# Performance work log

Hardware: AMD Instinct MI355X
Metric: run time of the kernel (lower is better)

## Reference

```python
import jax, jax.numpy as jnp
import numpy as np

B, T, IN, H = 64, 1024, 512, 512

def setup_inputs() -> dict:
    key = jax.random.key(0)
    k1, k2, k3, k4, k5 = jax.random.split(key, 5)
    s_w = 1.0 / np.sqrt(IN)
    s_u = 1.0 / np.sqrt(H)
    return {
        "X": jax.random.normal(k1, (B, T, IN), dtype=jnp.float32),
        "h_0": jnp.zeros((B, H), dtype=jnp.float32),
        "W_w": jax.random.uniform(k2, (H, IN), jnp.float32, -s_w, s_w),
        "W_b": jax.random.uniform(k3, (H,), jnp.float32, -s_w, s_w),
        "U_w": jax.random.uniform(k4, (H, H), jnp.float32, -s_u, s_u),
        "U_b": jax.random.uniform(k5, (H,), jnp.float32, -s_u, s_u),
    }

def reference(X, h_0, W_w, W_b, U_w, U_b):
    # Precompute input projection for all timesteps: [B,T,H]
    Wx = jnp.einsum('bti,hi->bth', X, W_w) + W_b
    Wx_t = jnp.swapaxes(Wx, 0, 1)  # [T,B,H] for scan

    def step(h_prev, wx_t):
        h_t = jnp.tanh(wx_t + h_prev @ U_w.T + U_b)
        return h_t, h_t

    _, H_seq = jax.lax.scan(step, h_0, Wx_t)  # [T,B,H]
    return jnp.swapaxes(H_seq, 0, 1)  # [B,T,H]
```

## Files before the change

kernel.cpp:

```cpp
#include <hip/hip_runtime.h>
#include <cstdint>
#include <cstddef>


#define T_STEPS 1024

using f16 = _Float16;
typedef f16  f16x2 __attribute__((ext_vector_type(2)));
typedef f16  f16x8 __attribute__((ext_vector_type(8)));
typedef float f32x4 __attribute__((ext_vector_type(4)));

#if __has_builtin(__builtin_amdgcn_fdot2)
#define FDOT2(a, b, c) __builtin_amdgcn_fdot2((a), (b), (c), false)
#else
static __device__ __forceinline__ float FDOT2(f16x2 a, f16x2 b, float c) {
    return c + (float)a[0] * (float)b[0] + (float)a[1] * (float)b[1];
}
#endif

static __device__ __forceinline__ f16x2 bcast_pair(int v) {
    return __builtin_bit_cast(f16x2, v);
}

__global__ __launch_bounds__(256, 2)
void gemm_wx(const float* __restrict__ X, const float* __restrict__ W,
             const float* __restrict__ Wb, float* __restrict__ out) {
    __shared__ __align__(16) char Al[128 * 128];
    __shared__ __align__(16) char Bl[128 * 128];

    const int tid  = threadIdx.x;
    const int lane = tid & 63;
    const int wid  = tid >> 6;
    const int wm   = wid & 1;
    const int wn   = wid >> 1;
    const int m0   = blockIdx.x * 128;
    const int n0   = blockIdx.y * 128;

    f32x4 acc[4][4] = {};

    for (int kt = 0; kt < 512; kt += 64) {
        __syncthreads();
#pragma unroll
        for (int i = 0; i < 4; ++i) {
            const int id   = tid + i * 256;
            const int row  = id >> 3;
            const int slot = id & 7;
            const float4* pa = reinterpret_cast<const float4*>(
                X + (size_t)(m0 + row) * 512 + kt + slot * 8);
            const float4* pb = reinterpret_cast<const float4*>(
                W + (size_t)(n0 + row) * 512 + kt + slot * 8);
            float4 a0 = pa[0], a1 = pa[1];
            float4 b0 = pb[0], b1 = pb[1];
            f16x8 va = { (f16)a0.x, (f16)a0.y, (f16)a0.z, (f16)a0.w,
                         (f16)a1.x, (f16)a1.y, (f16)a1.z, (f16)a1.w };
            f16x8 vb = { (f16)b0.x, (f16)b0.y, (f16)b0.z, (f16)b0.w,
                         (f16)b1.x, (f16)b1.y, (f16)b1.z, (f16)b1.w };
            const int cb = (slot * 16) ^ ((row & 7) << 4);
            *reinterpret_cast<f16x8*>(Al + row * 128 + cb) = va;
            *reinterpret_cast<f16x8*>(Bl + row * 128 + cb) = vb;
        }
        __syncthreads();

#pragma unroll
        for (int kk = 0; kk < 2; ++kk) {
            f16x8 af[4], bf[4];
#pragma unroll
            for (int mi = 0; mi < 4; ++mi) {
                const int r  = wm * 64 + mi * 16 + (lane & 15);
                const int cb = (kk * 64 + ((lane >> 4) * 16)) ^ ((r & 7) << 4);
                af[mi] = *reinterpret_cast<const f16x8*>(Al + r * 128 + cb);
            }
#pragma unroll
            for (int ni = 0; ni < 4; ++ni) {
                const int r  = wn * 64 + ni * 16 + (lane & 15);
                const int cb = (kk * 64 + ((lane >> 4) * 16)) ^ ((r & 7) << 4);
                bf[ni] = *reinterpret_cast<const f16x8*>(Bl + r * 128 + cb);
            }
#pragma unroll
            for (int mi = 0; mi < 4; ++mi)
#pragma unroll
                for (int ni = 0; ni < 4; ++ni)
                    acc[mi][ni] = __builtin_amdgcn_mfma_f32_16x16x32_f16(
                        af[mi], bf[ni], acc[mi][ni], 0, 0, 0);
        }
    }

#pragma unroll
    for (int ni = 0; ni < 4; ++ni) {
        const int col  = n0 + wn * 64 + ni * 16 + (lane & 15);
        const float bias = Wb[col];
#pragma unroll
        for (int mi = 0; mi < 4; ++mi) {
            const int rowb = m0 + wm * 64 + mi * 16 + ((lane >> 4) * 4);
#pragma unroll
            for (int e = 0; e < 4; ++e)
                out[(size_t)(rowb + e) * 512 + col] = acc[mi][ni][e] + bias;
        }
    }
}

#define KREG   448
#define NPREG  (KREG / 2)

__global__ __launch_bounds__(512, 2)
void rnn_scan(float* __restrict__ out, const float* __restrict__ h0,
              const float* __restrict__ Uw, const float* __restrict__ Ub) {
    const int tid  = threadIdx.x;
    const int b    = blockIdx.x;
    const int lane = tid & 63;

    f16x2 u[NPREG];
    {
        const float2* up = reinterpret_cast<const float2*>(Uw + (size_t)tid * 512);
#pragma unroll
        for (int p = 0; p < NPREG; ++p) {
            float2 v = up[p];
            u[p] = (f16x2){ (f16)v.x, (f16)v.y };
        }
    }
    const float ub = Ub[tid];

    __shared__ __align__(16) char utail[512 * 128];
    __shared__ __align__(16) char hb[2][1024];

    {
        const float4* tp = reinterpret_cast<const float4*>(Uw + (size_t)tid * 512 + KREG);
#pragma unroll
        for (int i = 0; i < 8; ++i) {
            float4 v0 = tp[2 * i], v1 = tp[2 * i + 1];
            f16x8 w = { (f16)v0.x, (f16)v0.y, (f16)v0.z, (f16)v0.w,
                        (f16)v1.x, (f16)v1.y, (f16)v1.z, (f16)v1.w };
            *reinterpret_cast<f16x8*>(utail + tid * 128 + ((16 * i) ^ ((tid & 7) << 4))) = w;
        }
    }

    float* const obase = out + (size_t)b * (T_STEPS * 512);

    *reinterpret_cast<f16*>(hb[0] + 2 * tid) = (f16)h0[b * 512 + tid];
    float wx = obase[tid];
    __syncthreads();

    for (int t = 0; t < T_STEPS; ++t) {
        const uint4 vh = *reinterpret_cast<const uint4*>(hb[t & 1] + 16 * lane);
        float wxn = 0.0f;
        if (t < T_STEPS - 1) wxn = obase[(size_t)(t + 1) * 512 + tid];

        float a0 = 0.f, a1 = 0.f, a2 = 0.f, a3 = 0.f;
#pragma unroll
        for (int p = 0; p < NPREG; p += 4) {
            const int ln = p >> 2;
            const int s0 = __builtin_amdgcn_readlane((int)vh.x, ln);
            const int s1 = __builtin_amdgcn_readlane((int)vh.y, ln);
            const int s2 = __builtin_amdgcn_readlane((int)vh.z, ln);
            const int s3 = __builtin_amdgcn_readlane((int)vh.w, ln);
            a0 = FDOT2(bcast_pair(s0), u[p + 0], a0);
            a1 = FDOT2(bcast_pair(s1), u[p + 1], a1);
            a2 = FDOT2(bcast_pair(s2), u[p + 2], a2);
            a3 = FDOT2(bcast_pair(s3), u[p + 3], a3);
        }
#pragma unroll
        for (int i = 0; i < 8; ++i) {
            const uint4 ut = *reinterpret_cast<const uint4*>(
                utail + tid * 128 + ((16 * i) ^ ((tid & 7) << 4)));
            const int ln = 56 + i;
            const int s0 = __builtin_amdgcn_readlane((int)vh.x, ln);
            const int s1 = __builtin_amdgcn_readlane((int)vh.y, ln);
            const int s2 = __builtin_amdgcn_readlane((int)vh.z, ln);
            const int s3 = __builtin_amdgcn_readlane((int)vh.w, ln);
            a0 = FDOT2(bcast_pair(s0), __builtin_bit_cast(f16x2, ut.x), a0);
            a1 = FDOT2(bcast_pair(s1), __builtin_bit_cast(f16x2, ut.y), a1);
            a2 = FDOT2(bcast_pair(s2), __builtin_bit_cast(f16x2, ut.z), a2);
            a3 = FDOT2(bcast_pair(s3), __builtin_bit_cast(f16x2, ut.w), a3);
        }

        const float a  = wx + ((a0 + a1) + (a2 + a3)) + ub;
        const float ax = fabsf(a);
        const float e  = __expf(2.0f * ax);
        const float r1 = 1.0f - 2.0f / (e + 1.0f);
        const float h  = copysignf(r1, a);

        *reinterpret_cast<f16*>(hb[(t + 1) & 1] + 2 * tid) = (f16)h;
        obase[(size_t)t * 512 + tid] = h;
        wx = wxn;
        __syncthreads();
    }
}

extern "C" void kernel_launch(void* const* d_in, const int* in_sizes, int n_in,
                              void* d_out, int out_size, void* d_ws, size_t ws_size,
                              hipStream_t stream) {
    const float* X  = (const float*)d_in[0];
    const float* h0 = (const float*)d_in[1];
    const float* Ww = (const float*)d_in[2];
    const float* Wb = (const float*)d_in[3];
    const float* Uw = (const float*)d_in[4];
    const float* Ub = (const float*)d_in[5];
    float* out = (float*)d_out;

    gemm_wx<<<dim3(512, 4), dim3(256), 0, stream>>>(X, Ww, Wb, out);
    rnn_scan<<<dim3(64), dim3(512), 0, stream>>>(out, h0, Uw, Ub);
}
```

Measured before the change: 2.335 ms.

## Rebalance U_w register/LDS split, fold U_b into GEMM bias, lighter barrier

Reduces the number of U_w pairs held in registers per thread from 224 to 208 and moves the remaining 48 pairs into LDS, stored in a column-major int layout that avoids conflicts. U_b is added into the GEMM epilogue bias so the scan no longer adds it. The __syncthreads at the end of each step becomes an inline s_waitcnt lgkmcnt(0) plus s_barrier, which skips waiting on the outstanding global stores. The intent is to cut register pressure and possible spills and to shorten the per-step sync; the cost is more LDS reads per step.

Result: no change. 2.338 ms (+0.2%).

```diff
diff --git a/kernel.cpp b/kernel.cpp
--- a/kernel.cpp
+++ b/kernel.cpp
@@ -4,6 +4,8 @@
 
 
 #define T_STEPS 1024
+#define NPV 208
+#define NTP 48
 
 using f16 = _Float16;
 typedef f16  f16x2 __attribute__((ext_vector_type(2)));
@@ -18,13 +20,22 @@
 }
 #endif
 
-static __device__ __forceinline__ f16x2 bcast_pair(int v) {
+static __device__ __forceinline__ f16x8 cvt8(float4 v0, float4 v1) {
+    return (f16x8){ (f16)v0.x, (f16)v0.y, (f16)v0.z, (f16)v0.w,
+                    (f16)v1.x, (f16)v1.y, (f16)v1.z, (f16)v1.w };
+}
+static __device__ __forceinline__ int pack2(float2 v) {
+    f16x2 p = { (f16)v.x, (f16)v.y };
+    return __builtin_bit_cast(int, p);
+}
+static __device__ __forceinline__ f16x2 asf16x2(int v) {
     return __builtin_bit_cast(f16x2, v);
 }
 
 __global__ __launch_bounds__(256, 2)
 void gemm_wx(const float* __restrict__ X, const float* __restrict__ W,
-             const float* __restrict__ Wb, float* __restrict__ out) {
+             const float* __restrict__ Wb, const float* __restrict__ Ub,
+             float* __restrict__ out) {
     __shared__ __align__(16) char Al[128 * 128];
     __shared__ __align__(16) char Bl[128 * 128];
 
@@ -49,12 +60,8 @@
                 X + (size_t)(m0 + row) * 512 + kt + slot * 8);
             const float4* pb = reinterpret_cast<const float4*>(
                 W + (size_t)(n0 + row) * 512 + kt + slot * 8);
-            float4 a0 = pa[0], a1 = pa[1];
-            float4 b0 = pb[0], b1 = pb[1];
-            f16x8 va = { (f16)a0.x, (f16)a0.y, (f16)a0.z, (f16)a0.w,
-                         (f16)a1.x, (f16)a1.y, (f16)a1.z, (f16)a1.w };
-            f16x8 vb = { (f16)b0.x, (f16)b0.y, (f16)b0.z, (f16)b0.w,
-                         (f16)b1.x, (f16)b1.y, (f16)b1.z, (f16)b1.w };
+            f16x8 va = cvt8(pa[0], pa[1]);
+            f16x8 vb = cvt8(pb[0], pb[1]);
             const int cb = (slot * 16) ^ ((row & 7) << 4);
             *reinterpret_cast<f16x8*>(Al + row * 128 + cb) = va;
             *reinterpret_cast<f16x8*>(Bl + row * 128 + cb) = vb;
@@ -88,7 +95,7 @@
 #pragma unroll
     for (int ni = 0; ni < 4; ++ni) {
         const int col  = n0 + wn * 64 + ni * 16 + (lane & 15);
-        const float bias = Wb[col];
+        const float bias = Wb[col] + Ub[col];
 #pragma unroll
         for (int mi = 0; mi < 4; ++mi) {
             const int rowb = m0 + wm * 64 + mi * 16 + ((lane >> 4) * 4);
@@ -99,44 +106,33 @@
     }
 }
 
-#define KREG   448
-#define NPREG  (KREG / 2)
-
 __global__ __launch_bounds__(512, 2)
 void rnn_scan(float* __restrict__ out, const float* __restrict__ h0,
-              const float* __restrict__ Uw, const float* __restrict__ Ub) {
+              const float* __restrict__ Uw) {
+    __shared__ __align__(16) int  Ut32[NTP * 512];
+    __shared__ __align__(16) char hb[2][1024];
+
     const int tid  = threadIdx.x;
     const int b    = blockIdx.x;
     const int lane = tid & 63;
 
-    f16x2 u[NPREG];
-    {
-        const float2* up = reinterpret_cast<const float2*>(Uw + (size_t)tid * 512);
+    const float2* up = reinterpret_cast<const float2*>(Uw + (size_t)tid * 512);
+    int uv[NPV];
 #pragma unroll
-        for (int p = 0; p < NPREG; ++p) {
-            float2 v = up[p];
-            u[p] = (f16x2){ (f16)v.x, (f16)v.y };
-        }
-    }
-    const float ub = Ub[tid];
-
-    __shared__ __align__(16) char utail[512 * 128];
-    __shared__ __align__(16) char hb[2][1024];
+    for (int p = 0; p < NPV; ++p)
+        uv[p] = pack2(up[p]);
 
     {
-        const float4* tp = reinterpret_cast<const float4*>(Uw + (size_t)tid * 512 + KREG);
+        const float2* tp = reinterpret_cast<const float2*>(
+            Uw + (size_t)tid * 512 + 416);
 #pragma unroll
-        for (int i = 0; i < 8; ++i) {
-            float4 v0 = tp[2 * i], v1 = tp[2 * i + 1];
-            f16x8 w = { (f16)v0.x, (f16)v0.y, (f16)v0.z, (f16)v0.w,
-                        (f16)v1.x, (f16)v1.y, (f16)v1.z, (f16)v1.w };
-            *reinterpret_cast<f16x8*>(utail + tid * 128 + ((16 * i) ^ ((tid & 7) << 4))) = w;
-        }
+        for (int c = 0; c < NTP; ++c)
+            Ut32[c * 512 + tid] = pack2(tp[c]);
     }
 
+    *reinterpret_cast<f16*>(hb[0] + 2 * tid) = (f16)h0[b * 512 + tid];
+
     float* const obase = out + (size_t)b * (T_STEPS * 512);
-
-    *reinterpret_cast<f16*>(hb[0] + 2 * tid) = (f16)h0[b * 512 + tid];
     float wx = obase[tid];
     __syncthreads();
 
@@ -146,43 +142,42 @@
         if (t < T_STEPS - 1) wxn = obase[(size_t)(t + 1) * 512 + tid];
 
         float a0 = 0.f, a1 = 0.f, a2 = 0.f, a3 = 0.f;
+
 #pragma unroll
-        for (int p = 0; p < NPREG; p += 4) {
-            const int ln = p >> 2;
-            const int s0 = __builtin_amdgcn_readlane((int)vh.x, ln);
-            const int s1 = __builtin_amdgcn_readlane((int)vh.y, ln);
-            const int s2 = __builtin_amdgcn_readlane((int)vh.z, ln);
-            const int s3 = __builtin_amdgcn_readlane((int)vh.w, ln);
-            a0 = FDOT2(bcast_pair(s0), u[p + 0], a0);
-            a1 = FDOT2(bcast_pair(s1), u[p + 1], a1);
-            a2 = FDOT2(bcast_pair(s2), u[p + 2], a2);
-            a3 = FDOT2(bcast_pair(s3), u[p + 3], a3);
+        for (int q4 = 0; q4 < NPV / 4; ++q4) {
+            const int h0_ = __builtin_amdgcn_readlane((int)vh.x, q4);
+            const int h1_ = __builtin_amdgcn_readlane((int)vh.y, q4);
+            const int h2_ = __builtin_amdgcn_readlane((int)vh.z, q4);
+            const int h3_ = __builtin_amdgcn_readlane((int)vh.w, q4);
+            a0 = FDOT2(asf16x2(uv[4 * q4 + 0]), asf16x2(h0_), a0);
+            a1 = FDOT2(asf16x2(uv[4 * q4 + 1]), asf16x2(h1_), a1);
+            a2 = FDOT2(asf16x2(uv[4 * q4 + 2]), asf16x2(h2_), a2);
+            a3 = FDOT2(asf16x2(uv[4 * q4 + 3]), asf16x2(h3_), a3);
         }
 #pragma unroll
-        for (int i = 0; i < 8; ++i) {
-            const uint4 ut = *reinterpret_cast<const uint4*>(
-                utail + tid * 128 + ((16 * i) ^ ((tid & 7) << 4)));
-            const int ln = 56 + i;
-            const int s0 = __builtin_amdgcn_readlane((int)vh.x, ln);
-            const int s1 = __builtin_amdgcn_readlane((int)vh.y, ln);
-            const int s2 = __builtin_amdgcn_readlane((int)vh.z, ln);
-            const int s3 = __builtin_amdgcn_readlane((int)vh.w, ln);
-            a0 = FDOT2(bcast_pair(s0), __builtin_bit_cast(f16x2, ut.x), a0);
-            a1 = FDOT2(bcast_pair(s1), __builtin_bit_cast(f16x2, ut.y), a1);
-            a2 = FDOT2(bcast_pair(s2), __builtin_bit_cast(f16x2, ut.z), a2);
-            a3 = FDOT2(bcast_pair(s3), __builtin_bit_cast(f16x2, ut.w), a3);
+        for (int c = 0; c < NTP; c += 4) {
+            const int ln  = NPV / 4 + (c >> 2);
+            const int h0_ = __builtin_amdgcn_readlane((int)vh.x, ln);
+            const int h1_ = __builtin_amdgcn_readlane((int)vh.y, ln);
+            const int h2_ = __builtin_amdgcn_readlane((int)vh.z, ln);
+            const int h3_ = __builtin_amdgcn_readlane((int)vh.w, ln);
+            a0 = FDOT2(asf16x2(Ut32[(c + 0) * 512 + tid]), asf16x2(h0_), a0);
+            a1 = FDOT2(asf16x2(Ut32[(c + 1) * 512 + tid]), asf16x2(h1_), a1);
+            a2 = FDOT2(asf16x2(Ut32[(c + 2) * 512 + tid]), asf16x2(h2_), a2);
+            a3 = FDOT2(asf16x2(Ut32[(c + 3) * 512 + tid]), asf16x2(h3_), a3);
         }
 
-        const float a  = wx + ((a0 + a1) + (a2 + a3)) + ub;
-        const float ax = fabsf(a);
+        const float aa = ((a0 + a1) + (a2 + a3)) + wx;
+        const float ax = fabsf(aa);
         const float e  = __expf(2.0f * ax);
         const float r1 = 1.0f - 2.0f / (e + 1.0f);
-        const float h  = copysignf(r1, a);
+        const float h  = copysignf(r1, aa);
 
+        obase[(size_t)t * 512 + tid] = h;
         *reinterpret_cast<f16*>(hb[(t + 1) & 1] + 2 * tid) = (f16)h;
-        obase[(size_t)t * 512 + tid] = h;
         wx = wxn;
-        __syncthreads();
+
+        asm volatile("s_waitcnt lgkmcnt(0)\n\ts_barrier" ::: "memory");
     }
 }
 
@@ -197,6 +192,6 @@
     const float* Ub = (const float*)d_in[5];
     float* out = (float*)d_out;
 
-    gemm_wx<<<dim3(512, 4), dim3(256), 0, stream>>>(X, Ww, Wb, out);
-    rnn_scan<<<dim3(64), dim3(512), 0, stream>>>(out, h0, Uw, Ub);
+    gemm_wx<<<dim3(512, 4), dim3(256), 0, stream>>>(X, Ww, Wb, Ub, out);
+    rnn_scan<<<dim3(64), dim3(512), 0, stream>>>(out, h0, Uw);
 }
```
